# Performance work log

Hardware: AMD Instinct MI355X
Metric: run time of the kernel (lower is better)

Reference implementation:

```python
import jax, jax.numpy as jnp
import numpy as np

H = 4096   # hidden_size
V = 4      # vocab_size (Dyck-2)
OUT = 4    # output_size
MS = 104   # memory_size (stack depth)
MD = 3     # memory_dim (stack element width)


def setup_inputs() -> dict:
    key = jax.random.key(0)
    ks = jax.random.split(key, 17)
    s = 1.0 / np.sqrt(H)
    f32 = jnp.float32
    return {
        "inp": jax.random.randint(ks[0], (1,), 0, H),
        "hidden0": jax.random.normal(ks[1], (1, 1, H), f32),
        "stack": jax.random.normal(ks[2], (MS, MD), f32),
        "emb": (jax.random.normal(ks[3], (H, V), f32) * s),      # nn.Embedding(H, V)
        "w_ih": (jax.random.normal(ks[4], (3 * H, V), f32) * s),  # GRU input weights
        "w_hh": (jax.random.normal(ks[5], (3 * H, H), f32) * s),  # GRU hidden weights
        "b_ih": (jax.random.normal(ks[6], (3 * H,), f32) * s),
        "b_hh": (jax.random.normal(ks[7], (3 * H,), f32) * s),
        "w_y": (jax.random.normal(ks[8], (OUT, H), f32) * s),
        "b_y": (jax.random.normal(ks[9], (OUT,), f32) * s),
        "w_n": (jax.random.normal(ks[10], (MD, H), f32) * s),
        "b_n": (jax.random.normal(ks[11], (MD,), f32) * s),
        "w_a": (jax.random.normal(ks[12], (2, H), f32) * s),
        "b_a": (jax.random.normal(ks[13], (2,), f32) * s),
        "w_sh": (jax.random.normal(ks[14], (H, MD), f32) * s),
        "b_sh": (jax.random.normal(ks[15], (H,), f32) * s),
    }


def reference(inp, hidden0, stack, emb, w_ih, w_hh, b_ih, b_hh,
              w_y, b_y, w_n, b_n, w_a, b_a, w_sh, b_sh):
    # embedded = embedding(inp).view(1,1,-1) -> work with flat (V,)
    x = emb[inp[0]]                                   # (V,)
    # hidden_bar = W_sh(stack[0]) + hidden0
    h_bar = (w_sh @ stack[0] + b_sh) + hidden0[0, 0]  # (H,)
    # one GRU step (PyTorch gate order: r, z, n)
    gi = w_ih @ x + b_ih                              # (3H,)
    gh = w_hh @ h_bar + b_hh                          # (3H,)
    i_r, i_z, i_n = jnp.split(gi, 3)
    h_r, h_z, h_n = jnp.split(gh, 3)
    r = jax.nn.sigmoid(i_r + h_r)
    z = jax.nn.sigmoid(i_z + h_z)
    n = jnp.tanh(i_n + r * h_n)
    h = (1.0 - z) * n + z * h_bar                     # (H,) = ht = hidden
    # heads
    output = jax.nn.sigmoid(w_y @ h + b_y).reshape(1, OUT)
    action = jax.nn.softmax(w_a @ h + b_a)            # (2,) push/pop weights
    new_elt = jax.nn.sigmoid(w_n @ h + b_n).reshape(1, MD)
    # differentiable stack update
    push_side = jnp.concatenate([new_elt, stack[:-1]], axis=0)          # (MS, MD)
    pop_side = jnp.concatenate([stack[1:], jnp.zeros((1, MD), stack.dtype)], axis=0)
    new_stack = action[0] * push_side + action[1] * pop_side
    hidden = h.reshape(1, 1, H)
    return output, hidden, new_stack
```

## Files before the change

kernel.cpp:

```cpp
#include <hip/hip_runtime.h>
#include <hip/hip_bf16.h>

#define H  4096
#define V  4
#define OUT_N 4
#define MS 104
#define MD 3

#define KPB 2
#define TPB (KPB * 3 * 64)

__device__ __forceinline__ float b2f(unsigned short u) {
    return __uint_as_float(((unsigned int)u) << 16);
}
__device__ __forceinline__ float ldf(const void* p, size_t i, bool is_f32) {
    return is_f32 ? ((const float*)p)[i] : b2f(((const unsigned short*)p)[i]);
}
__device__ __forceinline__ void stf(void* p, size_t i, bool is_f32, float v) {
    if (is_f32) ((float*)p)[i] = v;
    else        ((__hip_bfloat16*)p)[i] = __float2bfloat16(v);
}

__device__ __forceinline__ bool detect_f32(const void* w_hh) {
    const unsigned short* w = (const unsigned short*)w_hh;
    const int lane = threadIdx.x & 63;
    int bad = 0;
    #pragma unroll
    for (int i = 0; i < 16; ++i) {
        const float v = b2f(w[lane + (i << 6)]);
        if (!(fabsf(v) < 1.0e6f)) bad = 1;
    }
    return __ballot(bad) != 0ull;
}

__device__ __forceinline__ float dot8(uint4 a, float4 h0, float4 h1) {
    return __uint_as_float(a.x << 16)          * h0.x
         + __uint_as_float(a.x & 0xffff0000u)  * h0.y
         + __uint_as_float(a.y << 16)          * h0.z
         + __uint_as_float(a.y & 0xffff0000u)  * h0.w
         + __uint_as_float(a.z << 16)          * h1.x
         + __uint_as_float(a.z & 0xffff0000u)  * h1.y
         + __uint_as_float(a.w << 16)          * h1.z
         + __uint_as_float(a.w & 0xffff0000u)  * h1.w;
}

__global__ __launch_bounds__(TPB) void gru_fused_kernel(
    const int*  __restrict__ inp,  const void* __restrict__ emb,
    const void* __restrict__ w_ih, const void* __restrict__ w_hh,
    const void* __restrict__ b_ih, const void* __restrict__ b_hh,
    const void* __restrict__ w_sh, const void* __restrict__ b_sh,
    const void* __restrict__ hidden0, const void* __restrict__ stack,
    float* __restrict__ h_f32, void* __restrict__ out) {
    const bool f32 = detect_f32(w_hh);
    const int t = threadIdx.x;
    const int wave = t >> 6, lane = t & 63;
    const int k0 = blockIdx.x * KPB;

    __shared__ float hb_lds[H];
    __shared__ float red[KPB][3];

    const float s0 = ldf(stack, 0, f32);
    const float s1 = ldf(stack, 1, f32);
    const float s2 = ldf(stack, 2, f32);
    for (int j = t; j < H; j += TPB) {
        hb_lds[j] = ldf(w_sh, (size_t)j * 3 + 0, f32) * s0
                  + ldf(w_sh, (size_t)j * 3 + 1, f32) * s1
                  + ldf(w_sh, (size_t)j * 3 + 2, f32) * s2
                  + ldf(b_sh, j, f32) + ldf(hidden0, j, f32);
    }
    __syncthreads();

    const int g  = wave % 3;
    const int kk = wave / 3;
    const int row = g * H + k0 + kk;

    float acc = 0.f;
    if (f32) {
        const float4* W  = (const float4*)w_hh + (size_t)row * (H / 4);
        const float4* HB = (const float4*)hb_lds;
        #pragma unroll 4
        for (int it = 0; it < H / 256; ++it) {
            const int i = (it << 6) + lane;
            const float4 a = W[i], hb = HB[i];
            acc += a.x * hb.x + a.y * hb.y + a.z * hb.z + a.w * hb.w;
        }
    } else {
        const uint4*  W  = (const uint4*)w_hh + (size_t)row * (H / 8);
        const float4* HB = (const float4*)hb_lds;
        #pragma unroll 4
        for (int it = 0; it < H / 512; ++it) {
            const int i = (it << 6) + lane;
            acc += dot8(W[i], HB[2 * i], HB[2 * i + 1]);
        }
    }
    #pragma unroll
    for (int off = 32; off > 0; off >>= 1) acc += __shfl_down(acc, off);
    if (lane == 0) red[kk][g] = acc;
    __syncthreads();

    if (t < KPB) {
        const int k = k0 + t;
        const float sr = red[t][0], sz = red[t][1], sn = red[t][2];

        const int idx = inp[0];
        float x[V];
        #pragma unroll
        for (int c = 0; c < V; ++c) x[c] = ldf(emb, (size_t)idx * V + c, f32);

        float gi[3];
        #pragma unroll
        for (int gg = 0; gg < 3; ++gg) {
            float a = ldf(b_ih, (size_t)(k + gg * H), f32);
            #pragma unroll
            for (int c = 0; c < V; ++c)
                a += ldf(w_ih, (size_t)(k + gg * H) * V + c, f32) * x[c];
            gi[gg] = a;
        }
        const float ghr = sr + ldf(b_hh, (size_t)k,           f32);
        const float ghz = sz + ldf(b_hh, (size_t)(k + H),     f32);
        const float ghn = sn + ldf(b_hh, (size_t)(k + 2 * H), f32);

        const float r = 1.f / (1.f + expf(-(gi[0] + ghr)));
        const float z = 1.f / (1.f + expf(-(gi[1] + ghz)));
        const float n = tanhf(gi[2] + r * ghn);
        const float hk = (1.f - z) * n + z * hb_lds[k];

        h_f32[k] = hk;
        stf(out, (size_t)(OUT_N + k), f32, hk);
    }
}

__global__ __launch_bounds__(1024) void heads_kernel(
    const float* __restrict__ h,
    const void* __restrict__ w_y, const void* __restrict__ b_y,
    const void* __restrict__ w_a, const void* __restrict__ b_a,
    const void* __restrict__ w_n, const void* __restrict__ b_n,
    const void* __restrict__ stack, const void* __restrict__ w_hh,
    void* __restrict__ out) {
    const bool f32 = detect_f32(w_hh);
    const int t = threadIdx.x, wave = t >> 6, lane = t & 63;

    __shared__ float scal[9];
    if (wave < 9) {
        const void* base; size_t row;
        if (wave < 4)      { base = w_y; row = (size_t)wave * H; }
        else if (wave < 6) { base = w_a; row = (size_t)(wave - 4) * H; }
        else               { base = w_n; row = (size_t)(wave - 6) * H; }

        float acc = 0.f;
        if (f32) {
            const float4* W  = (const float4*)((const float*)base + row);
            const float4* Hv = (const float4*)h;
            #pragma unroll 4
            for (int it = 0; it < H / 256; ++it) {
                const int i = (it << 6) + lane;
                const float4 a = W[i], hb = Hv[i];
                acc += a.x * hb.x + a.y * hb.y + a.z * hb.z + a.w * hb.w;
            }
        } else {
            const uint4*  W  = (const uint4*)((const unsigned short*)base + row);
            const float4* Hv = (const float4*)h;
            #pragma unroll 2
            for (int it = 0; it < H / 512; ++it) {
                const int i = (it << 6) + lane;
                acc += dot8(W[i], Hv[2 * i], Hv[2 * i + 1]);
            }
        }
        #pragma unroll
        for (int off = 32; off > 0; off >>= 1) acc += __shfl_down(acc, off);
        if (lane == 0) scal[wave] = acc;
    }
    __syncthreads();

    __shared__ float act0, act1, ne[MD];
    if (t == 0) {
        const float a0 = scal[4] + ldf(b_a, 0, f32);
        const float a1 = scal[5] + ldf(b_a, 1, f32);
        const float m  = fmaxf(a0, a1);
        const float e0 = expf(a0 - m), e1 = expf(a1 - m);
        const float inv = 1.f / (e0 + e1);
        act0 = e0 * inv; act1 = e1 * inv;
    }
    if (t < OUT_N)
        stf(out, (size_t)t, f32,
            1.f / (1.f + expf(-(scal[t] + ldf(b_y, t, f32)))));
    if (t < MD)
        ne[t] = 1.f / (1.f + expf(-(scal[6 + t] + ldf(b_n, t, f32))));
    __syncthreads();

    const float a0 = act0, a1 = act1;
    for (int idx = t; idx < MS * MD; idx += 1024) {
        const int i = idx / MD;
        const int d = idx - i * MD;
        const float push = (i == 0)      ? ne[d] : ldf(stack, (size_t)(idx - MD), f32);
        const float pop  = (i == MS - 1) ? 0.f   : ldf(stack, (size_t)(idx + MD), f32);
        stf(out, (size_t)(OUT_N + H + idx), f32, a0 * push + a1 * pop);
    }
}

extern "C" void kernel_launch(void* const* d_in, const int* in_sizes, int n_in,
                              void* d_out, int out_size, void* d_ws, size_t ws_size,
                              hipStream_t stream) {
    const int* inp      = (const int*)d_in[0];
    const void* hidden0 = d_in[1];
    const void* stack   = d_in[2];
    const void* emb     = d_in[3];
    const void* w_ih    = d_in[4];
    const void* w_hh    = d_in[5];
    const void* b_ih    = d_in[6];
    const void* b_hh    = d_in[7];
    const void* w_y     = d_in[8];
    const void* b_y     = d_in[9];
    const void* w_n     = d_in[10];
    const void* b_n     = d_in[11];
    const void* w_a     = d_in[12];
    const void* b_a     = d_in[13];
    const void* w_sh    = d_in[14];
    const void* b_sh    = d_in[15];

    float* h = (float*)d_ws;

    gru_fused_kernel<<<H / KPB, TPB, 0, stream>>>(
        inp, emb, w_ih, w_hh, b_ih, b_hh, w_sh, b_sh, hidden0, stack, h, d_out);
    heads_kernel<<<1, 1024, 0, stream>>>(h, w_y, b_y, w_a, b_a, w_n, b_n,
                                         stack, w_hh, d_out);
}
```

Baseline: 321.4 us.

## Precompute h_bar once and fuse heads into GRU via last-block atomic

Adds a small kernel that computes h_bar once, so the 2048 GRU blocks no longer each recompute it from w_sh, b_sh and hidden0. The GRU blocks just copy h_bar into LDS. The heads and stack update move into the GRU kernel and run in whichever block finishes last, detected with a threadfence plus an atomic counter; this drops the separate heads launch. Unroll factors are also raised. The cost is a serialized tail in one 384-thread block, plus the counter reset done in the first kernel.

Result: slower. 375.5 us (+16.8%).

```diff
diff --git a/kernel.cpp b/kernel.cpp
--- a/kernel.cpp
+++ b/kernel.cpp
@@ -9,6 +9,7 @@
 
 #define KPB 2
 #define TPB (KPB * 3 * 64)
+#define NBLK (H / KPB)
 
 __device__ __forceinline__ float b2f(unsigned short u) {
     return __uint_as_float(((unsigned int)u) << 16);
@@ -44,29 +45,46 @@
          + __uint_as_float(a.w & 0xffff0000u)  * h1.w;
 }
 
-__global__ __launch_bounds__(TPB) void gru_fused_kernel(
+__global__ __launch_bounds__(256) void hbar_kernel(
+    const void* __restrict__ w_sh, const void* __restrict__ b_sh,
+    const void* __restrict__ hidden0, const void* __restrict__ stack,
+    const void* __restrict__ w_hh, float* __restrict__ h_bar,
+    int* __restrict__ counter) {
+    const bool f32 = detect_f32(w_hh);
+    if (blockIdx.x == 0 && threadIdx.x == 0) *counter = 0;
+    const float s0 = ldf(stack, 0, f32);
+    const float s1 = ldf(stack, 1, f32);
+    const float s2 = ldf(stack, 2, f32);
+    const int j = blockIdx.x * 256 + threadIdx.x;
+    h_bar[j] = ldf(w_sh, (size_t)j * 3 + 0, f32) * s0
+             + ldf(w_sh, (size_t)j * 3 + 1, f32) * s1
+             + ldf(w_sh, (size_t)j * 3 + 2, f32) * s2
+             + ldf(b_sh, j, f32) + ldf(hidden0, j, f32);
+}
+
+__global__ __launch_bounds__(TPB) void gru_kernel(
     const int*  __restrict__ inp,  const void* __restrict__ emb,
     const void* __restrict__ w_ih, const void* __restrict__ w_hh,
     const void* __restrict__ b_ih, const void* __restrict__ b_hh,
-    const void* __restrict__ w_sh, const void* __restrict__ b_sh,
-    const void* __restrict__ hidden0, const void* __restrict__ stack,
-    float* __restrict__ h_f32, void* __restrict__ out) {
+    const float* __restrict__ h_bar,
+    const void* __restrict__ w_y, const void* __restrict__ b_y,
+    const void* __restrict__ w_a, const void* __restrict__ b_a,
+    const void* __restrict__ w_n, const void* __restrict__ b_n,
+    const void* __restrict__ stack,
+    float* __restrict__ h_f32, int* __restrict__ counter,
+    void* __restrict__ out) {
     const bool f32 = detect_f32(w_hh);
-    const int t = threadIdx.x;
-    const int wave = t >> 6, lane = t & 63;
+    const int t = threadIdx.x, wave = t >> 6, lane = t & 63;
     const int k0 = blockIdx.x * KPB;
 
-    __shared__ float hb_lds[H];
+    __shared__ float hb[H];
     __shared__ float red[KPB][3];
-
-    const float s0 = ldf(stack, 0, f32);
-    const float s1 = ldf(stack, 1, f32);
-    const float s2 = ldf(stack, 2, f32);
-    for (int j = t; j < H; j += TPB) {
-        hb_lds[j] = ldf(w_sh, (size_t)j * 3 + 0, f32) * s0
-                  + ldf(w_sh, (size_t)j * 3 + 1, f32) * s1
-                  + ldf(w_sh, (size_t)j * 3 + 2, f32) * s2
-                  + ldf(b_sh, j, f32) + ldf(hidden0, j, f32);
+    __shared__ int   isLast;
+
+    {
+        const float4* src = (const float4*)h_bar;
+        float4* dst = (float4*)hb;
+        for (int i = t; i < H / 4; i += TPB) dst[i] = src[i];
     }
     __syncthreads();
 
@@ -77,17 +95,17 @@
     float acc = 0.f;
     if (f32) {
         const float4* W  = (const float4*)w_hh + (size_t)row * (H / 4);
-        const float4* HB = (const float4*)hb_lds;
-        #pragma unroll 4
+        const float4* HB = (const float4*)hb;
+        #pragma unroll 8
         for (int it = 0; it < H / 256; ++it) {
             const int i = (it << 6) + lane;
-            const float4 a = W[i], hb = HB[i];
-            acc += a.x * hb.x + a.y * hb.y + a.z * hb.z + a.w * hb.w;
+            const float4 a = W[i], b = HB[i];
+            acc += a.x * b.x + a.y * b.y + a.z * b.z + a.w * b.w;
         }
     } else {
         const uint4*  W  = (const uint4*)w_hh + (size_t)row * (H / 8);
-        const float4* HB = (const float4*)hb_lds;
-        #pragma unroll 4
+        const float4* HB = (const float4*)hb;
+        #pragma unroll 8
         for (int it = 0; it < H / 512; ++it) {
             const int i = (it << 6) + lane;
             acc += dot8(W[i], HB[2 * i], HB[2 * i + 1]);
@@ -98,77 +116,79 @@
     if (lane == 0) red[kk][g] = acc;
     __syncthreads();
 
-    if (t < KPB) {
-        const int k = k0 + t;
-        const float sr = red[t][0], sz = red[t][1], sn = red[t][2];
-
+    if (t == 0) {
         const int idx = inp[0];
         float x[V];
         #pragma unroll
         for (int c = 0; c < V; ++c) x[c] = ldf(emb, (size_t)idx * V + c, f32);
 
-        float gi[3];
         #pragma unroll
-        for (int gg = 0; gg < 3; ++gg) {
-            float a = ldf(b_ih, (size_t)(k + gg * H), f32);
+        for (int kk2 = 0; kk2 < KPB; ++kk2) {
+            const int k = k0 + kk2;
+            float gi[3];
             #pragma unroll
-            for (int c = 0; c < V; ++c)
-                a += ldf(w_ih, (size_t)(k + gg * H) * V + c, f32) * x[c];
-            gi[gg] = a;
-        }
-        const float ghr = sr + ldf(b_hh, (size_t)k,           f32);
-        const float ghz = sz + ldf(b_hh, (size_t)(k + H),     f32);
-        const float ghn = sn + ldf(b_hh, (size_t)(k + 2 * H), f32);
-
-        const float r = 1.f / (1.f + expf(-(gi[0] + ghr)));
-        const float z = 1.f / (1.f + expf(-(gi[1] + ghz)));
-        const float n = tanhf(gi[2] + r * ghn);
-        const float hk = (1.f - z) * n + z * hb_lds[k];
-
-        h_f32[k] = hk;
-        stf(out, (size_t)(OUT_N + k), f32, hk);
-    }
-}
-
-__global__ __launch_bounds__(1024) void heads_kernel(
-    const float* __restrict__ h,
-    const void* __restrict__ w_y, const void* __restrict__ b_y,
-    const void* __restrict__ w_a, const void* __restrict__ b_a,
-    const void* __restrict__ w_n, const void* __restrict__ b_n,
-    const void* __restrict__ stack, const void* __restrict__ w_hh,
-    void* __restrict__ out) {
-    const bool f32 = detect_f32(w_hh);
-    const int t = threadIdx.x, wave = t >> 6, lane = t & 63;
+            for (int gg = 0; gg < 3; ++gg) {
+                float a = ldf(b_ih, (size_t)(k + gg * H), f32);
+                #pragma unroll
+                for (int c = 0; c < V; ++c)
+                    a += ldf(w_ih, (size_t)(k + gg * H) * V + c, f32) * x[c];
+                gi[gg] = a;
+            }
+            const float ghr = red[kk2][0] + ldf(b_hh, (size_t)k,           f32);
+            const float ghz = red[kk2][1] + ldf(b_hh, (size_t)(k + H),     f32);
+            const float ghn = red[kk2][2] + ldf(b_hh, (size_t)(k + 2 * H), f32);
+
+            const float r = 1.f / (1.f + expf(-(gi[0] + ghr)));
+            const float z = 1.f / (1.f + expf(-(gi[1] + ghz)));
+            const float n = tanhf(gi[2] + r * ghn);
+            const float hk = (1.f - z) * n + z * hb[k];
+
+            h_f32[k] = hk;
+            stf(out, (size_t)(OUT_N + k), f32, hk);
+        }
+        __threadfence();
+        isLast = (atomicAdd(counter, 1) == NBLK - 1) ? 1 : 0;
+    }
+    __syncthreads();
+    if (!isLast) return;
+
+    __threadfence();
+    {
+        const float4* src = (const float4*)h_f32;
+        float4* dst = (float4*)hb;
+        for (int i = t; i < H / 4; i += TPB) dst[i] = src[i];
+    }
+    __syncthreads();
 
     __shared__ float scal[9];
-    if (wave < 9) {
-        const void* base; size_t row;
-        if (wave < 4)      { base = w_y; row = (size_t)wave * H; }
-        else if (wave < 6) { base = w_a; row = (size_t)(wave - 4) * H; }
-        else               { base = w_n; row = (size_t)(wave - 6) * H; }
-
-        float acc = 0.f;
+    for (int r = wave; r < 9; r += TPB / 64) {
+        const void* base; size_t ro;
+        if (r < 4)      { base = w_y; ro = (size_t)r * H; }
+        else if (r < 6) { base = w_a; ro = (size_t)(r - 4) * H; }
+        else            { base = w_n; ro = (size_t)(r - 6) * H; }
+
+        float a2 = 0.f;
         if (f32) {
-            const float4* W  = (const float4*)((const float*)base + row);
-            const float4* Hv = (const float4*)h;
-            #pragma unroll 4
+            const float4* W  = (const float4*)((const float*)base + ro);
+            const float4* Hv = (const float4*)hb;
+            #pragma unroll 8
             for (int it = 0; it < H / 256; ++it) {
                 const int i = (it << 6) + lane;
-                const float4 a = W[i], hb = Hv[i];
-                acc += a.x * hb.x + a.y * hb.y + a.z * hb.z + a.w * hb.w;
+                const float4 w4 = W[i], hv = Hv[i];
+                a2 += w4.x * hv.x + w4.y * hv.y + w4.z * hv.z + w4.w * hv.w;
             }
         } else {
-            const uint4*  W  = (const uint4*)((const unsigned short*)base + row);
-            const float4* Hv = (const float4*)h;
-            #pragma unroll 2
+            const uint4*  W  = (const uint4*)((const unsigned short*)base + ro);
+            const float4* Hv = (const float4*)hb;
+            #pragma unroll 8
             for (int it = 0; it < H / 512; ++it) {
                 const int i = (it << 6) + lane;
-                acc += dot8(W[i], Hv[2 * i], Hv[2 * i + 1]);
+                a2 += dot8(W[i], Hv[2 * i], Hv[2 * i + 1]);
             }
         }
         #pragma unroll
-        for (int off = 32; off > 0; off >>= 1) acc += __shfl_down(acc, off);
-        if (lane == 0) scal[wave] = acc;
+        for (int off = 32; off > 0; off >>= 1) a2 += __shfl_down(a2, off);
+        if (lane == 0) scal[r] = a2;
     }
     __syncthreads();
 
@@ -189,7 +209,7 @@
     __syncthreads();
 
     const float a0 = act0, a1 = act1;
-    for (int idx = t; idx < MS * MD; idx += 1024) {
+    for (int idx = t; idx < MS * MD; idx += TPB) {
         const int i = idx / MD;
         const int d = idx - i * MD;
         const float push = (i == 0)      ? ne[d] : ldf(stack, (size_t)(idx - MD), f32);
@@ -218,10 +238,13 @@
     const void* w_sh    = d_in[14];
     const void* b_sh    = d_in[15];
 
-    float* h = (float*)d_ws;
-
-    gru_fused_kernel<<<H / KPB, TPB, 0, stream>>>(
-        inp, emb, w_ih, w_hh, b_ih, b_hh, w_sh, b_sh, hidden0, stack, h, d_out);
-    heads_kernel<<<1, 1024, 0, stream>>>(h, w_y, b_y, w_a, b_a, w_n, b_n,
-                                         stack, w_hh, d_out);
-}
+    float* h_bar   = (float*)d_ws;
+    float* h       = h_bar + H;
+    int*   counter = (int*)(h + H);
+
+    hbar_kernel<<<H / 256, 256, 0, stream>>>(w_sh, b_sh, hidden0, stack,
+                                             w_hh, h_bar, counter);
+    gru_kernel<<<NBLK, TPB, 0, stream>>>(
+        inp, emb, w_ih, w_hh, b_ih, b_hh, h_bar,
+        w_y, b_y, w_a, b_a, w_n, b_n, stack, h, counter, d_out);
+}
```

## Split GRU matvec into column-partitioned partial sums with atomic accumulation

Applied to the files above, without the earlier changes.

Replaces the fused GRU kernel, where each block recomputed the full hidden_bar vector into LDS and dotted whole rows, with a split-K scheme. Each block now handles a 512-column slice of w_hh, computing only its own slice of hidden_bar in registers, and reduces 4 rows at a time with atomicAdd into a zeroed workspace. Separate zero and gate kernels follow. This removes the redundant per-block hidden_bar recomputation and LDS staging, at the cost of two extra launches, global atomics and non-deterministic summation order.

Measured after the change: 331.2 us. 1.03x slower.

```diff
diff --git a/kernel.cpp b/kernel.cpp
--- a/kernel.cpp
+++ b/kernel.cpp
@@ -7,8 +7,11 @@
 #define MS 104
 #define MD 3
 
-#define KPB 2
-#define TPB (KPB * 3 * 64)
+#define R3H (3 * H)
+#define PW  512
+#define P   (H / PW)
+#define BPP 256
+#define RPW (R3H / (BPP * 4))
 
 __device__ __forceinline__ float b2f(unsigned short u) {
     return __uint_as_float(((unsigned int)u) << 16);
@@ -44,90 +47,145 @@
          + __uint_as_float(a.w & 0xffff0000u)  * h1.w;
 }
 
-__global__ __launch_bounds__(TPB) void gru_fused_kernel(
+__device__ __forceinline__ float wave_reduce(float a) {
+    #pragma unroll
+    for (int off = 32; off > 0; off >>= 1) a += __shfl_down(a, off);
+    return a;
+}
+
+__global__ __launch_bounds__(256) void zero_kernel(float* __restrict__ acc) {
+    acc[blockIdx.x * 256 + threadIdx.x] = 0.f;
+}
+
+__global__ __launch_bounds__(256) void partial_kernel(
+    const void* __restrict__ w_hh,
+    const void* __restrict__ w_sh, const void* __restrict__ b_sh,
+    const void* __restrict__ hidden0, const void* __restrict__ stack,
+    float* __restrict__ acc) {
+    const bool f32 = detect_f32(w_hh);
+    const int t = threadIdx.x, wave = t >> 6, lane = t & 63;
+    const int p     = blockIdx.x / BPP;
+    const int rbase = ((blockIdx.x % BPP) * 4 + wave) * RPW;
+
+    const float s0 = ldf(stack, 0, f32);
+    const float s1 = ldf(stack, 1, f32);
+    const float s2 = ldf(stack, 2, f32);
+    const int j0 = p * PW + lane * 8;
+    float hs[8];
+    #pragma unroll
+    for (int e = 0; e < 8; ++e) {
+        const int j = j0 + e;
+        hs[e] = ldf(w_sh, (size_t)j * 3 + 0, f32) * s0
+              + ldf(w_sh, (size_t)j * 3 + 1, f32) * s1
+              + ldf(w_sh, (size_t)j * 3 + 2, f32) * s2
+              + ldf(b_sh, j, f32) + ldf(hidden0, j, f32);
+    }
+    const float4 h0 = make_float4(hs[0], hs[1], hs[2], hs[3]);
+    const float4 h1 = make_float4(hs[4], hs[5], hs[6], hs[7]);
+
+    if (f32) {
+        const float4* W = (const float4*)w_hh;
+        #pragma unroll
+        for (int c = 0; c < RPW / 4; ++c) {
+            const int r = rbase + c * 4;
+            const size_t base = ((size_t)r * H + p * PW) / 4 + lane * 2;
+            const size_t strd = H / 4;
+            const float4 a0 = W[base];            const float4 b0 = W[base + 1];
+            const float4 a1 = W[base + strd];     const float4 b1 = W[base + strd + 1];
+            const float4 a2 = W[base + 2*strd];   const float4 b2 = W[base + 2*strd + 1];
+            const float4 a3 = W[base + 3*strd];   const float4 b3 = W[base + 3*strd + 1];
+            float v0 = a0.x*h0.x + a0.y*h0.y + a0.z*h0.z + a0.w*h0.w
+                     + b0.x*h1.x + b0.y*h1.y + b0.z*h1.z + b0.w*h1.w;
+            float v1 = a1.x*h0.x + a1.y*h0.y + a1.z*h0.z + a1.w*h0.w
+                     + b1.x*h1.x + b1.y*h1.y + b1.z*h1.z + b1.w*h1.w;
+            float v2 = a2.x*h0.x + a2.y*h0.y + a2.z*h0.z + a2.w*h0.w
+                     + b2.x*h1.x + b2.y*h1.y + b2.z*h1.z + b2.w*h1.w;
+            float v3 = a3.x*h0.x + a3.y*h0.y + a3.z*h0.z + a3.w*h0.w
+                     + b3.x*h1.x + b3.y*h1.y + b3.z*h1.z + b3.w*h1.w;
+            v0 = wave_reduce(v0); v1 = wave_reduce(v1);
+            v2 = wave_reduce(v2); v3 = wave_reduce(v3);
+            if (lane == 0) {
+                atomicAdd(&acc[r],     v0);
+                atomicAdd(&acc[r + 1], v1);
+                atomicAdd(&acc[r + 2], v2);
+                atomicAdd(&acc[r + 3], v3);
+            }
+        }
+    } else {
+        const uint4* W = (const uint4*)w_hh;
+        #pragma unroll
+        for (int c = 0; c < RPW / 4; ++c) {
+            const int r = rbase + c * 4;
+            const size_t base = ((size_t)r * H + p * PW) / 8 + lane;
+            const size_t strd = H / 8;
+            const uint4 a0 = W[base];
+            const uint4 a1 = W[base + strd];
+            const uint4 a2 = W[base + 2 * strd];
+            const uint4 a3 = W[base + 3 * strd];
+            float v0 = dot8(a0, h0, h1);
+            float v1 = dot8(a1, h0, h1);
+            float v2 = dot8(a2, h0, h1);
+            float v3 = dot8(a3, h0, h1);
+            v0 = wave_reduce(v0); v1 = wave_reduce(v1);
+            v2 = wave_reduce(v2); v3 = wave_reduce(v3);
+            if (lane == 0) {
+                atomicAdd(&acc[r],     v0);
+                atomicAdd(&acc[r + 1], v1);
+                atomicAdd(&acc[r + 2], v2);
+                atomicAdd(&acc[r + 3], v3);
+            }
+        }
+    }
+}
+
+__global__ __launch_bounds__(256) void gates_kernel(
     const int*  __restrict__ inp,  const void* __restrict__ emb,
     const void* __restrict__ w_ih, const void* __restrict__ w_hh,
     const void* __restrict__ b_ih, const void* __restrict__ b_hh,
     const void* __restrict__ w_sh, const void* __restrict__ b_sh,
     const void* __restrict__ hidden0, const void* __restrict__ stack,
+    const float* __restrict__ acc,
     float* __restrict__ h_f32, void* __restrict__ out) {
     const bool f32 = detect_f32(w_hh);
-    const int t = threadIdx.x;
-    const int wave = t >> 6, lane = t & 63;
-    const int k0 = blockIdx.x * KPB;
-
-    __shared__ float hb_lds[H];
-    __shared__ float red[KPB][3];
+    const int k = blockIdx.x * 256 + threadIdx.x;
+
+    const float sr = acc[k];
+    const float sz = acc[k + H];
+    const float sn = acc[k + 2 * H];
 
     const float s0 = ldf(stack, 0, f32);
     const float s1 = ldf(stack, 1, f32);
     const float s2 = ldf(stack, 2, f32);
-    for (int j = t; j < H; j += TPB) {
-        hb_lds[j] = ldf(w_sh, (size_t)j * 3 + 0, f32) * s0
-                  + ldf(w_sh, (size_t)j * 3 + 1, f32) * s1
-                  + ldf(w_sh, (size_t)j * 3 + 2, f32) * s2
-                  + ldf(b_sh, j, f32) + ldf(hidden0, j, f32);
-    }
-    __syncthreads();
-
-    const int g  = wave % 3;
-    const int kk = wave / 3;
-    const int row = g * H + k0 + kk;
-
-    float acc = 0.f;
-    if (f32) {
-        const float4* W  = (const float4*)w_hh + (size_t)row * (H / 4);
-        const float4* HB = (const float4*)hb_lds;
-        #pragma unroll 4
-        for (int it = 0; it < H / 256; ++it) {
-            const int i = (it << 6) + lane;
-            const float4 a = W[i], hb = HB[i];
-            acc += a.x * hb.x + a.y * hb.y + a.z * hb.z + a.w * hb.w;
-        }
-    } else {
-        const uint4*  W  = (const uint4*)w_hh + (size_t)row * (H / 8);
-        const float4* HB = (const float4*)hb_lds;
-        #pragma unroll 4
-        for (int it = 0; it < H / 512; ++it) {
-            const int i = (it << 6) + lane;
-            acc += dot8(W[i], HB[2 * i], HB[2 * i + 1]);
-        }
-    }
-    #pragma unroll
-    for (int off = 32; off > 0; off >>= 1) acc += __shfl_down(acc, off);
-    if (lane == 0) red[kk][g] = acc;
-    __syncthreads();
-
-    if (t < KPB) {
-        const int k = k0 + t;
-        const float sr = red[t][0], sz = red[t][1], sn = red[t][2];
-
-        const int idx = inp[0];
-        float x[V];
+    const float hbk = ldf(w_sh, (size_t)k * 3 + 0, f32) * s0
+                    + ldf(w_sh, (size_t)k * 3 + 1, f32) * s1
+                    + ldf(w_sh, (size_t)k * 3 + 2, f32) * s2
+                    + ldf(b_sh, k, f32) + ldf(hidden0, k, f32);
+
+    const int idx = inp[0];
+    float x[V];
+    #pragma unroll
+    for (int c = 0; c < V; ++c) x[c] = ldf(emb, (size_t)idx * V + c, f32);
+
+    float gi[3];
+    #pragma unroll
+    for (int g = 0; g < 3; ++g) {
+        float a = ldf(b_ih, (size_t)(k + g * H), f32);
         #pragma unroll
-        for (int c = 0; c < V; ++c) x[c] = ldf(emb, (size_t)idx * V + c, f32);
-
-        float gi[3];
-        #pragma unroll
-        for (int gg = 0; gg < 3; ++gg) {
-            float a = ldf(b_ih, (size_t)(k + gg * H), f32);
-            #pragma unroll
-            for (int c = 0; c < V; ++c)
-                a += ldf(w_ih, (size_t)(k + gg * H) * V + c, f32) * x[c];
-            gi[gg] = a;
-        }
-        const float ghr = sr + ldf(b_hh, (size_t)k,           f32);
-        const float ghz = sz + ldf(b_hh, (size_t)(k + H),     f32);
-        const float ghn = sn + ldf(b_hh, (size_t)(k + 2 * H), f32);
-
-        const float r = 1.f / (1.f + expf(-(gi[0] + ghr)));
-        const float z = 1.f / (1.f + expf(-(gi[1] + ghz)));
-        const float n = tanhf(gi[2] + r * ghn);
-        const float hk = (1.f - z) * n + z * hb_lds[k];
-
-        h_f32[k] = hk;
-        stf(out, (size_t)(OUT_N + k), f32, hk);
-    }
+        for (int c = 0; c < V; ++c)
+            a += ldf(w_ih, (size_t)(k + g * H) * V + c, f32) * x[c];
+        gi[g] = a;
+    }
+    const float ghr = sr + ldf(b_hh, (size_t)k,           f32);
+    const float ghz = sz + ldf(b_hh, (size_t)(k + H),     f32);
+    const float ghn = sn + ldf(b_hh, (size_t)(k + 2 * H), f32);
+
+    const float r = 1.f / (1.f + expf(-(gi[0] + ghr)));
+    const float z = 1.f / (1.f + expf(-(gi[1] + ghz)));
+    const float n = tanhf(gi[2] + r * ghn);
+    const float hk = (1.f - z) * n + z * hbk;
+
+    h_f32[k] = hk;
+    stf(out, (size_t)(OUT_N + k), f32, hk);
 }
 
 __global__ __launch_bounds__(1024) void heads_kernel(
@@ -166,8 +224,7 @@
                 acc += dot8(W[i], Hv[2 * i], Hv[2 * i + 1]);
             }
         }
-        #pragma unroll
-        for (int off = 32; off > 0; off >>= 1) acc += __shfl_down(acc, off);
+        acc = wave_reduce(acc);
         if (lane == 0) scal[wave] = acc;
     }
     __syncthreads();
@@ -218,10 +275,15 @@
     const void* w_sh    = d_in[14];
     const void* b_sh    = d_in[15];
 
-    float* h = (float*)d_ws;
-
-    gru_fused_kernel<<<H / KPB, TPB, 0, stream>>>(
-        inp, emb, w_ih, w_hh, b_ih, b_hh, w_sh, b_sh, hidden0, stack, h, d_out);
+    float* acc = (float*)d_ws;
+    float* h   = acc + R3H;
+
+    zero_kernel<<<R3H / 256, 256, 0, stream>>>(acc);
+    partial_kernel<<<P * BPP, 256, 0, stream>>>(w_hh, w_sh, b_sh, hidden0,
+                                                stack, acc);
+    gates_kernel<<<H / 256, 256, 0, stream>>>(inp, emb, w_ih, w_hh, b_ih, b_hh,
+                                              w_sh, b_sh, hidden0, stack,
+                                              acc, h, d_out);
     heads_kernel<<<1, 1024, 0, stream>>>(h, w_y, b_y, w_a, b_a, w_n, b_n,
                                          stack, w_hh, d_out);
 }
```

## Split h_bar precompute into its own kernel and use atomic-counter gate combine

Applied to the files above, without the earlier changes.

Computes h_bar once in a separate small kernel instead of having each of the 2048 blocks recompute all 4096 entries of it. The row kernel now gives each wave one of the 3H rows of w_hh and issues all of its loads up front into registers. Each wave writes its partial result to global memory. The last of the three gate rows per hidden unit, detected with an atomic counter, then applies the GRU nonlinearity. This trades redundant per-block recomputation for an extra launch and global atomics and fences.

After: 948.9 us. 195% more time.

```diff
diff --git a/kernel.cpp b/kernel.cpp
--- a/kernel.cpp
+++ b/kernel.cpp
@@ -6,9 +6,7 @@
 #define OUT_N 4
 #define MS 104
 #define MD 3
-
-#define KPB 2
-#define TPB (KPB * 3 * 64)
+#define R3H (3 * H)
 
 __device__ __forceinline__ float b2f(unsigned short u) {
     return __uint_as_float(((unsigned int)u) << 16);
@@ -43,90 +41,107 @@
          + __uint_as_float(a.w << 16)          * h1.z
          + __uint_as_float(a.w & 0xffff0000u)  * h1.w;
 }
-
-__global__ __launch_bounds__(TPB) void gru_fused_kernel(
+__device__ __forceinline__ float dot4(float4 a, float4 b) {
+    return a.x * b.x + a.y * b.y + a.z * b.z + a.w * b.w;
+}
+__device__ __forceinline__ float wave_reduce(float a) {
+    #pragma unroll
+    for (int off = 32; off > 0; off >>= 1) a += __shfl_down(a, off);
+    return a;
+}
+
+__global__ __launch_bounds__(256) void hbar_kernel(
+    const void* __restrict__ w_sh, const void* __restrict__ b_sh,
+    const void* __restrict__ hidden0, const void* __restrict__ stack,
+    const void* __restrict__ w_hh, float* __restrict__ h_bar,
+    int* __restrict__ cnt) {
+    const bool f32 = detect_f32(w_hh);
+    const float s0 = ldf(stack, 0, f32);
+    const float s1 = ldf(stack, 1, f32);
+    const float s2 = ldf(stack, 2, f32);
+    const int j = blockIdx.x * 256 + threadIdx.x;
+    cnt[j] = 0;
+    h_bar[j] = ldf(w_sh, (size_t)j * 3 + 0, f32) * s0
+             + ldf(w_sh, (size_t)j * 3 + 1, f32) * s1
+             + ldf(w_sh, (size_t)j * 3 + 2, f32) * s2
+             + ldf(b_sh, j, f32) + ldf(hidden0, j, f32);
+}
+
+__global__ __launch_bounds__(256) void rows_kernel(
     const int*  __restrict__ inp,  const void* __restrict__ emb,
     const void* __restrict__ w_ih, const void* __restrict__ w_hh,
     const void* __restrict__ b_ih, const void* __restrict__ b_hh,
-    const void* __restrict__ w_sh, const void* __restrict__ b_sh,
-    const void* __restrict__ hidden0, const void* __restrict__ stack,
+    const float* __restrict__ h_bar,
+    float* __restrict__ gh, int* __restrict__ cnt,
     float* __restrict__ h_f32, void* __restrict__ out) {
     const bool f32 = detect_f32(w_hh);
-    const int t = threadIdx.x;
-    const int wave = t >> 6, lane = t & 63;
-    const int k0 = blockIdx.x * KPB;
-
-    __shared__ float hb_lds[H];
-    __shared__ float red[KPB][3];
-
-    const float s0 = ldf(stack, 0, f32);
-    const float s1 = ldf(stack, 1, f32);
-    const float s2 = ldf(stack, 2, f32);
-    for (int j = t; j < H; j += TPB) {
-        hb_lds[j] = ldf(w_sh, (size_t)j * 3 + 0, f32) * s0
-                  + ldf(w_sh, (size_t)j * 3 + 1, f32) * s1
-                  + ldf(w_sh, (size_t)j * 3 + 2, f32) * s2
-                  + ldf(b_sh, j, f32) + ldf(hidden0, j, f32);
+    const int t = threadIdx.x, wave = t >> 6, lane = t & 63;
+    const int r = blockIdx.x * 4 + wave;
+    const int k = r & (H - 1);
+
+    __shared__ float4 hb4[H / 4];
+    {
+        const float4* src = (const float4*)h_bar;
+        #pragma unroll
+        for (int i = 0; i < 4; ++i) hb4[t + 256 * i] = src[t + 256 * i];
     }
     __syncthreads();
-
-    const int g  = wave % 3;
-    const int kk = wave / 3;
-    const int row = g * H + k0 + kk;
 
     float acc = 0.f;
     if (f32) {
-        const float4* W  = (const float4*)w_hh + (size_t)row * (H / 4);
-        const float4* HB = (const float4*)hb_lds;
-        #pragma unroll 4
-        for (int it = 0; it < H / 256; ++it) {
-            const int i = (it << 6) + lane;
-            const float4 a = W[i], hb = HB[i];
-            acc += a.x * hb.x + a.y * hb.y + a.z * hb.z + a.w * hb.w;
+        const float4* W = (const float4*)w_hh + (size_t)r * (H / 4);
+        float4 a[16];
+        #pragma unroll
+        for (int i = 0; i < 16; ++i) a[i] = W[i * 64 + lane];
+        #pragma unroll
+        for (int i = 0; i < 16; ++i) acc += dot4(a[i], hb4[i * 64 + lane]);
+    } else {
+        const uint4* W = (const uint4*)w_hh + (size_t)r * (H / 8);
+        uint4 a[8];
+        #pragma unroll
+        for (int i = 0; i < 8; ++i) a[i] = W[i * 64 + lane];
+        #pragma unroll
+        for (int i = 0; i < 8; ++i)
+            acc += dot8(a[i], hb4[i * 128 + lane * 2], hb4[i * 128 + lane * 2 + 1]);
+    }
+    acc = wave_reduce(acc);
+
+    if (lane == 0) {
+        gh[r] = acc;
+        __threadfence();
+        const int old = atomicAdd(&cnt[k], 1);
+        if (old == 2) {
+            __threadfence();
+            const float sr = gh[k];
+            const float sz = gh[k + H];
+            const float sn = gh[k + 2 * H];
+
+            const int idx = inp[0];
+            float x[V];
+            #pragma unroll
+            for (int c = 0; c < V; ++c) x[c] = ldf(emb, (size_t)idx * V + c, f32);
+
+            float gi[3];
+            #pragma unroll
+            for (int gg = 0; gg < 3; ++gg) {
+                float a = ldf(b_ih, (size_t)(k + gg * H), f32);
+                #pragma unroll
+                for (int c = 0; c < V; ++c)
+                    a += ldf(w_ih, (size_t)(k + gg * H) * V + c, f32) * x[c];
+                gi[gg] = a;
+            }
+            const float ghr = sr + ldf(b_hh, (size_t)k,           f32);
+            const float ghz = sz + ldf(b_hh, (size_t)(k + H),     f32);
+            const float ghn = sn + ldf(b_hh, (size_t)(k + 2 * H), f32);
+
+            const float rr = 1.f / (1.f + expf(-(gi[0] + ghr)));
+            const float zz = 1.f / (1.f + expf(-(gi[1] + ghz)));
+            const float nn = tanhf(gi[2] + rr * ghn);
+            const float hk = (1.f - zz) * nn + zz * h_bar[k];
+
+            h_f32[k] = hk;
+            stf(out, (size_t)(OUT_N + k), f32, hk);
         }
-    } else {
-        const uint4*  W  = (const uint4*)w_hh + (size_t)row * (H / 8);
-        const float4* HB = (const float4*)hb_lds;
-        #pragma unroll 4
-        for (int it = 0; it < H / 512; ++it) {
-            const int i = (it << 6) + lane;
-            acc += dot8(W[i], HB[2 * i], HB[2 * i + 1]);
-        }
-    }
-    #pragma unroll
-    for (int off = 32; off > 0; off >>= 1) acc += __shfl_down(acc, off);
-    if (lane == 0) red[kk][g] = acc;
-    __syncthreads();
-
-    if (t < KPB) {
-        const int k = k0 + t;
-        const float sr = red[t][0], sz = red[t][1], sn = red[t][2];
-
-        const int idx = inp[0];
-        float x[V];
-        #pragma unroll
-        for (int c = 0; c < V; ++c) x[c] = ldf(emb, (size_t)idx * V + c, f32);
-
-        float gi[3];
-        #pragma unroll
-        for (int gg = 0; gg < 3; ++gg) {
-            float a = ldf(b_ih, (size_t)(k + gg * H), f32);
-            #pragma unroll
-            for (int c = 0; c < V; ++c)
-                a += ldf(w_ih, (size_t)(k + gg * H) * V + c, f32) * x[c];
-            gi[gg] = a;
-        }
-        const float ghr = sr + ldf(b_hh, (size_t)k,           f32);
-        const float ghz = sz + ldf(b_hh, (size_t)(k + H),     f32);
-        const float ghn = sn + ldf(b_hh, (size_t)(k + 2 * H), f32);
-
-        const float r = 1.f / (1.f + expf(-(gi[0] + ghr)));
-        const float z = 1.f / (1.f + expf(-(gi[1] + ghz)));
-        const float n = tanhf(gi[2] + r * ghn);
-        const float hk = (1.f - z) * n + z * hb_lds[k];
-
-        h_f32[k] = hk;
-        stf(out, (size_t)(OUT_N + k), f32, hk);
     }
 }
 
@@ -154,8 +169,7 @@
             #pragma unroll 4
             for (int it = 0; it < H / 256; ++it) {
                 const int i = (it << 6) + lane;
-                const float4 a = W[i], hb = Hv[i];
-                acc += a.x * hb.x + a.y * hb.y + a.z * hb.z + a.w * hb.w;
+                acc += dot4(W[i], Hv[i]);
             }
         } else {
             const uint4*  W  = (const uint4*)((const unsigned short*)base + row);
@@ -166,8 +180,7 @@
                 acc += dot8(W[i], Hv[2 * i], Hv[2 * i + 1]);
             }
         }
-        #pragma unroll
-        for (int off = 32; off > 0; off >>= 1) acc += __shfl_down(acc, off);
+        acc = wave_reduce(acc);
         if (lane == 0) scal[wave] = acc;
     }
     __syncthreads();
@@ -218,10 +231,15 @@
     const void* w_sh    = d_in[14];
     const void* b_sh    = d_in[15];
 
-    float* h = (float*)d_ws;
-
-    gru_fused_kernel<<<H / KPB, TPB, 0, stream>>>(
-        inp, emb, w_ih, w_hh, b_ih, b_hh, w_sh, b_sh, hidden0, stack, h, d_out);
+    float* gh    = (float*)d_ws;
+    int*   cnt   = (int*)(gh + R3H);
+    float* h_bar = (float*)(cnt + H);
+    float* h     = h_bar + H;
+
+    hbar_kernel<<<H / 256, 256, 0, stream>>>(w_sh, b_sh, hidden0, stack,
+                                             w_hh, h_bar, cnt);
+    rows_kernel<<<R3H / 4, 256, 0, stream>>>(inp, emb, w_ih, w_hh, b_ih, b_hh,
+                                             h_bar, gh, cnt, h, d_out);
     heads_kernel<<<1, 1024, 0, stream>>>(h, w_y, b_y, w_a, b_a, w_n, b_n,
                                          stack, w_hh, d_out);
 }
```
